# Kernel tuning notes

Hardware: AMD Instinct MI355X
Metric: run time of the kernel (lower is better)

## Reference

```python
import jax, jax.numpy as jnp
import numpy as np

H = 8  # number of heads


def setup_inputs() -> dict:
    key = jax.random.key(0)
    ks = jax.random.split(key, 8)
    B, L, S, D, P = 4, 2048, 2048, 1024, 1024
    sc = 0.02
    return {
        "queries": jax.random.normal(ks[0], (B, L, D), jnp.float32),
        "keys": jax.random.normal(ks[1], (B, S, D), jnp.float32),
        "values": jax.random.normal(ks[2], (B, S, D), jnp.float32),
        "Wq": jax.random.normal(ks[3], (D, P), jnp.float32) * sc,
        "bq": jnp.zeros((P,), jnp.float32),
        "Wk": jax.random.normal(ks[4], (D, P), jnp.float32) * sc,
        "bk": jnp.zeros((P,), jnp.float32),
        "Wv": jax.random.normal(ks[5], (D, P), jnp.float32) * sc,
        "bv": jnp.zeros((P,), jnp.float32),
        "Wo": jax.random.normal(ks[6], (P, D), jnp.float32) * sc,
        "bo": jnp.zeros((D,), jnp.float32),
    }


def reference(queries, keys, values, Wq, bq, Wk, bk, Wv, bv, Wo, bo):
    B, L, _ = queries.shape
    S = keys.shape[1]
    # linear projections, split into heads: [B, T, H, E]
    q = (queries @ Wq + bq).reshape(B, L, H, -1)
    k = (keys @ Wk + bk).reshape(B, S, H, -1)
    v = (values @ Wv + bv).reshape(B, S, H, -1)
    E = q.shape[-1]
    scale = 1.0 / jnp.sqrt(jnp.float32(E))
    scores = jnp.einsum("blhe,bshe->bhls", q, k)
    A = jax.nn.softmax(scale * scores, axis=-1)  # dropout is identity at eval
    V = jnp.einsum("bhls,bshd->blhd", A, v)
    out = V.reshape(B, L, -1)
    return out @ Wo + bo
```

## Files before the change

### kernel.cpp

```cpp
#include <hip/hip_runtime.h>
#include <hip/hip_bf16.h>
#include <cstdint>

typedef __attribute__((ext_vector_type(4))) float f32x4;
typedef __attribute__((ext_vector_type(16))) float f32x16;
typedef __attribute__((ext_vector_type(8))) __bf16 bf16x8;
typedef __attribute__((ext_vector_type(4))) unsigned u32x4;

#define SCALE_Q 0.12751744f

__device__ __forceinline__ short bf16b(float f) {
  unsigned u = __builtin_bit_cast(unsigned, f);
  unsigned r = (u + 0x7fffu + ((u >> 16) & 1u)) >> 16;
  return (short)r;
}

__device__ __forceinline__ unsigned packbf(float lo, float hi) {
  unsigned r;
  asm("v_cvt_pk_bf16_f32 %0, %1, %2" : "=v"(r) : "v"(lo), "v"(hi));
  return r;
}

__device__ __forceinline__ float exp2fast(float x) {
  float r;
  asm("v_exp_f32 %0, %1" : "=v"(r) : "v"(x));
  return r;
}

__device__ __forceinline__ f32x4 mfma16(bf16x8 a, bf16x8 b, f32x4 c) {
  return __builtin_amdgcn_mfma_f32_16x16x32_bf16(a, b, c, 0, 0, 0);
}
__device__ __forceinline__ f32x16 mfma32(bf16x8 a, bf16x8 b, f32x16 c) {
  return __builtin_amdgcn_mfma_f32_32x32x16_bf16(a, b, c, 0, 0, 0);
}

__device__ __forceinline__ void async16(void* lds, const void* g) {
  __builtin_amdgcn_global_load_lds(
      (const __attribute__((address_space(1))) unsigned int*)g,
      (__attribute__((address_space(3))) unsigned int*)lds, 16, 0, 0);
}

__global__ void cvt_x(const float* __restrict__ q, const float* __restrict__ k,
                      const float* __restrict__ v, short* __restrict__ out) {
  const float* src = (blockIdx.y == 0) ? q : (blockIdx.y == 1 ? k : v);
  short* dst = out + (size_t)blockIdx.y * 8388608;
  size_t i = (size_t)blockIdx.x * 256 + threadIdx.x;
  float4 f = reinterpret_cast<const float4*>(src)[i];
  short4 o;
  o.x = bf16b(f.x); o.y = bf16b(f.y); o.z = bf16b(f.z); o.w = bf16b(f.w);
  reinterpret_cast<short4*>(dst)[i] = o;
}

__global__ void cvt_w(const float* __restrict__ Wq, const float* __restrict__ Wk,
                      const float* __restrict__ Wv, const float* __restrict__ Wo,
                      short* __restrict__ out) {
  int z = blockIdx.z;
  const float* W = (z == 0) ? Wq : (z == 1) ? Wk : (z == 2) ? Wv : Wo;
  float scale = (z == 0) ? SCALE_Q : 1.0f;
  __shared__ float t[64][65];
  int n0 = blockIdx.x * 64, k0 = blockIdx.y * 64;
  int c = threadIdx.x & 63, r0 = threadIdx.x >> 6;
#pragma unroll
  for (int rr = 0; rr < 16; ++rr) {
    int r = rr * 4 + r0;
    t[r][c] = W[(size_t)(k0 + r) * 1024 + n0 + c];
  }
  __syncthreads();
  short* dst = out + (size_t)z * 1048576;
#pragma unroll
  for (int rr = 0; rr < 16; ++rr) {
    int r = rr * 4 + r0;
    dst[(size_t)(n0 + r) * 1024 + k0 + c] = bf16b(t[c][r] * scale);
  }
}

__global__ __launch_bounds__(256, 4) void gemm128(
    const short* __restrict__ Ab, const short* __restrict__ WT,
    const float* __restrict__ bq, const float* __restrict__ bk,
    const float* __restrict__ bv, const float* __restrict__ bo,
    short* __restrict__ Qg, short* __restrict__ Kg, short* __restrict__ Vtg,
    float* __restrict__ Out, int zbase, int nwg) {
  __shared__ __align__(16) short LDSbuf[16384];
  short* As = LDSbuf;
  short* Bs = LDSbuf + 8192;

  int cpx = nwg >> 3;
  int swz = ((int)blockIdx.x & 7) * cpx + ((int)blockIdx.x >> 3);
  int z, rem;
  if (zbase == 0) { z = swz >> 9; rem = swz & 511; }
  else { z = 3; rem = swz; }
  int m0 = (rem >> 3) * 128, n0 = (rem & 7) * 128;

  const short* A = (zbase == 0) ? Ab + (size_t)z * 8388608 : Ab;
  const short* Bn = WT + (size_t)z * 1048576;

  int tid = threadIdx.x;
  int lane = tid & 63, wave = tid >> 6;
  int wr = wave >> 1, wc = wave & 1, l15 = lane & 15, lg = lane >> 4;

  f32x4 acc[4][4];
#pragma unroll
  for (int mt = 0; mt < 4; ++mt)
#pragma unroll
    for (int nt = 0; nt < 4; ++nt) acc[mt][nt] = f32x4{0.f, 0.f, 0.f, 0.f};

  for (int k0 = 0; k0 < 1024; k0 += 64) {
#pragma unroll
    for (int i = 0; i < 4; ++i) {
      int r = (tid >> 3) + i * 32, c = tid & 7;
      int gc = c ^ (r & 7);
      async16((char*)As + i * 4096 + tid * 16,
              (const char*)A + ((size_t)(m0 + r) * 1024 + k0) * 2 + gc * 16);
      async16((char*)Bs + i * 4096 + tid * 16,
              (const char*)Bn + ((size_t)(n0 + r) * 1024 + k0) * 2 + gc * 16);
    }
    __syncthreads();
#pragma unroll
    for (int kk = 0; kk < 2; ++kk) {
      bf16x8 a[4], b[4];
#pragma unroll
      for (int mt = 0; mt < 4; ++mt) {
        int r = wr * 64 + mt * 16 + l15;
        a[mt] = *(const bf16x8*)((const char*)As + r * 128 +
                                 ((lg * 16 + kk * 64) ^ ((r & 7) << 4)));
      }
#pragma unroll
      for (int nt = 0; nt < 4; ++nt) {
        int r = wc * 64 + nt * 16 + l15;
        b[nt] = *(const bf16x8*)((const char*)Bs + r * 128 +
                                 ((lg * 16 + kk * 64) ^ ((r & 7) << 4)));
      }
#pragma unroll
      for (int mt = 0; mt < 4; ++mt)
#pragma unroll
        for (int nt = 0; nt < 4; ++nt)
          acc[mt][nt] = mfma16(a[mt], b[nt], acc[mt][nt]);
    }
    __syncthreads();
  }

  if (z == 2) {
    unsigned* Lt = (unsigned*)LDSbuf;
    int b_ = m0 >> 11, h_ = n0 >> 7;
    size_t bh = (size_t)b_ * 8 + h_;
    int sbase = m0 & 2047;
#pragma unroll
    for (int p = 0; p < 2; ++p) {
      if (wc == p) {
#pragma unroll
        for (int nt = 0; nt < 4; ++nt) {
          int el = nt * 16 + l15;
          float bb = bv[n0 + p * 64 + el];
#pragma unroll
          for (int mt = 0; mt < 4; ++mt) {
            int sw = wr * 32 + mt * 8 + lg * 2;
            unsigned lo = packbf(acc[mt][nt][0] + bb, acc[mt][nt][1] + bb);
            unsigned hi = packbf(acc[mt][nt][2] + bb, acc[mt][nt][3] + bb);
            *(uint2*)&Lt[el * 68 + sw] = make_uint2(lo, hi);
          }
        }
      }
      asm volatile("s_waitcnt lgkmcnt(0)" ::: "memory");
      __builtin_amdgcn_s_barrier();
      {
        int row = tid >> 2, ch = tid & 3;
        int e_ = p * 64 + row;
        int sx = ((e_ >> 1) & 7) << 3;
#pragma unroll
        for (int i = 0; i < 4; ++i) {
          int w = ch * 16 + i * 4;
          u32x4 val = *(const u32x4*)&Lt[row * 68 + w];
          int sb = (sbase + w * 2) ^ sx;
          *(u32x4*)&Vtg[(bh * 128 + e_) * 2048 + sb] = val;
        }
      }
      asm volatile("s_waitcnt lgkmcnt(0)" ::: "memory");
      __builtin_amdgcn_s_barrier();
    }
  } else {
#pragma unroll
    for (int mt = 0; mt < 4; ++mt)
#pragma unroll
      for (int nt = 0; nt < 4; ++nt) {
        int n = n0 + wc * 64 + nt * 16 + l15;
        float bb = (z == 0)   ? bq[n] * SCALE_Q
                   : (z == 1) ? bk[n]
                              : bo[n];
#pragma unroll
        for (int j = 0; j < 4; ++j) {
          int m = m0 + wr * 64 + mt * 16 + lg * 4 + j;
          float cv = acc[mt][nt][j] + bb;
          if (z == 3) {
            Out[(size_t)m * 1024 + n] = cv;
          } else {
            short o = bf16b(cv);
            int s_ = m & 2047, b_ = m >> 11, h_ = n >> 7, e_ = n & 127;
            size_t bh = (size_t)b_ * 8 + h_;
            if (z == 0)
              Qg[(bh * 2048 + s_) * 128 + e_] = o;
            else
              Kg[(bh * 2048 + s_) * 128 + (e_ ^ ((s_ & 15) << 3))] = o;
          }
        }
      }
  }
}

__global__ __launch_bounds__(256, 2) void attn(const short* __restrict__ Qg,
                                               const short* __restrict__ Kg,
                                               const short* __restrict__ Vtg,
                                               short* __restrict__ Ctx) {
  __shared__ short Ks[2][8192];
  __shared__ short Vs[2][8192];
  int tid = threadIdx.x;
  int lane = tid & 63, wave = tid >> 6;
  int l31 = lane & 31, h = lane >> 5;
  int bid = blockIdx.x;
  int swz = (bid & 7) * 64 + (bid >> 3);
  int bh = swz >> 4, qb = swz & 15;
  int qbase = qb * 128 + wave * 32;
  const short* Qp = Qg + (size_t)bh * 2048 * 128;
  const char* Kbase = (const char*)(Kg + (size_t)bh * 2048 * 128);
  const char* Vbase = (const char*)(Vtg + (size_t)bh * 128 * 2048);

  auto stage = [&](int t, int buf) {
    int s0 = t * 64;
    char* kd = (char*)&Ks[buf][0];
    char* vd = (char*)&Vs[buf][0];
#pragma unroll
    for (int i = 0; i < 4; ++i)
      async16(kd + i * 4096 + tid * 16,
              Kbase + (size_t)s0 * 256 + i * 4096 + tid * 16);
#pragma unroll
    for (int i = 0; i < 4; ++i) {
      int e = i * 32 + 2 * (tid >> 4) + ((tid >> 3) & 1);
      async16(vd + i * 4096 + tid * 16,
              Vbase + (size_t)e * 4096 + s0 * 2 + (tid & 7) * 16);
    }
  };

  stage(0, 0);

  bf16x8 qa[8];
  const short* qrow = Qp + (size_t)(qbase + l31) * 128 + h * 8;
#pragma unroll
  for (int ksl = 0; ksl < 8; ++ksl) qa[ksl] = *(const bf16x8*)(qrow + ksl * 16);

  f32x16 acc[4];
#pragma unroll
  for (int i = 0; i < 4; ++i)
#pragma unroll
    for (int r = 0; r < 16; ++r) acc[i][r] = 0.f;
  float mrun = -1e30f, lrun = 0.f;

  int swK = (l31 & 15) << 3;
  int swV = ((l31 >> 1) & 7) << 3;

  for (int t = 0; t < 32; ++t) {
    int cur = t & 1;
    if (t < 31) {
      stage(t + 1, cur ^ 1);
      asm volatile("s_waitcnt vmcnt(8)" ::: "memory");
    } else {
      asm volatile("s_waitcnt vmcnt(0)" ::: "memory");
    }
    __builtin_amdgcn_s_barrier();

    const short* Kc = Ks[cur];
    const short* Vc = Vs[cur];

    f32x16 st0, st1;
#pragma unroll
    for (int r = 0; r < 16; ++r) { st0[r] = 0.f; st1[r] = 0.f; }
    __builtin_amdgcn_s_setprio(1);
#pragma unroll
    for (int ksl = 0; ksl < 8; ++ksl) {
      int col = (ksl * 16 + h * 8) ^ swK;
      bf16x8 ka0 = *(const bf16x8*)&Kc[l31 * 128 + col];
      bf16x8 ka1 = *(const bf16x8*)&Kc[(32 + l31) * 128 + col];
      st0 = mfma32(ka0, qa[ksl], st0);
      st1 = mfma32(ka1, qa[ksl], st1);
    }
    __builtin_amdgcn_s_setprio(0);

    float m8[8];
#pragma unroll
    for (int r = 0; r < 8; ++r)
      m8[r] = fmaxf(fmaxf(st0[r], st0[r + 8]), fmaxf(st1[r], st1[r + 8]));
    float mx = fmaxf(fmaxf(fmaxf(m8[0], m8[1]), fmaxf(m8[2], m8[3])),
                     fmaxf(fmaxf(m8[4], m8[5]), fmaxf(m8[6], m8[7])));
    mx = fmaxf(mx, __shfl_xor(mx, 32));
    int skip = __all(mx - mrun <= 7.0f);
    float mn = mrun, sf = 1.f;
    if (!skip) {
      mn = fmaxf(mrun, mx);
      sf = exp2fast(mrun - mn);
      mrun = mn;
    }
#pragma unroll
    for (int r = 0; r < 16; ++r) { st0[r] = exp2fast(st0[r] - mn); }
#pragma unroll
    for (int r = 0; r < 16; ++r) { st1[r] = exp2fast(st1[r] - mn); }
    float s8[8];
#pragma unroll
    for (int r = 0; r < 8; ++r)
      s8[r] = (st0[r] + st0[r + 8]) + (st1[r] + st1[r + 8]);
    float rs = ((s8[0] + s8[1]) + (s8[2] + s8[3])) +
               ((s8[4] + s8[5]) + (s8[6] + s8[7]));
    rs += __shfl_xor(rs, 32);
    if (!skip) {
      lrun = lrun * sf + rs;
#pragma unroll
      for (int reg = 0; reg < 16; ++reg) {
        float s4 = __shfl(sf, (reg & 3) + 8 * (reg >> 2) + 4 * h);
#pragma unroll
        for (int nte = 0; nte < 4; ++nte) acc[nte][reg] *= s4;
      }
    } else {
      lrun += rs;
    }

    unsigned w0[8], w1[8];
#pragma unroll
    for (int m = 0; m < 8; ++m) {
      w0[m] = packbf(st0[2 * m], st0[2 * m + 1]);
      w1[m] = packbf(st1[2 * m], st1[2 * m + 1]);
    }
    bf16x8 pa[4];
#pragma unroll
    for (int ks = 0; ks < 4; ++ks) {
      const unsigned* w = (ks & 2) ? w1 : w0;
      int mb = (ks & 1) * 4;
      unsigned a0 = w[mb], b0 = w[mb + 2];
      unsigned a1 = w[mb + 1], b1 = w[mb + 3];
      asm volatile("v_permlane32_swap_b32 %0, %1" : "+v"(a0), "+v"(b0));
      asm volatile("v_permlane32_swap_b32 %0, %1" : "+v"(a1), "+v"(b1));
      u32x4 tt;
      tt[0] = a0; tt[1] = a1; tt[2] = b0; tt[3] = b1;
      pa[ks] = __builtin_bit_cast(bf16x8, tt);
    }

    __builtin_amdgcn_s_setprio(1);
#pragma unroll
    for (int nte = 0; nte < 4; ++nte) {
      int rbase = (nte * 16 + (l31 >> 1)) * 128 + (lane & 1) * 64;
#pragma unroll
      for (int ks = 0; ks < 4; ++ks) {
        int colk = (ks * 16 + h * 8) ^ swV;
        bf16x8 vb = *(const bf16x8*)&Vc[rbase + colk];
        acc[nte] = mfma32(pa[ks], vb, acc[nte]);
      }
    }
    __builtin_amdgcn_s_setprio(0);
    __builtin_amdgcn_s_barrier();
  }

  float inv = 1.0f / lrun;
  int b_ = bh >> 3, h_ = bh & 7;
#pragma unroll
  for (int reg = 0; reg < 16; ++reg) {
    int qr = (reg & 3) + 8 * (reg >> 2) + 4 * h;
    float iq = __shfl(inv, qr);
    int q = qbase + qr;
    short* orow = Ctx + (((size_t)b_ * 2048 + q) * 8 + h_) * 128;
#pragma unroll
    for (int nte = 0; nte < 4; ++nte)
      orow[nte * 32 + l31] = bf16b(acc[nte][reg] * iq);
  }
}

extern "C" void kernel_launch(void* const* d_in, const int* in_sizes, int n_in,
                              void* d_out, int out_size, void* d_ws, size_t ws_size,
                              hipStream_t stream) {
  const float* q = (const float*)d_in[0];
  const float* k = (const float*)d_in[1];
  const float* v = (const float*)d_in[2];
  const float* Wq = (const float*)d_in[3];
  const float* bq = (const float*)d_in[4];
  const float* Wk = (const float*)d_in[5];
  const float* bk = (const float*)d_in[6];
  const float* Wv = (const float*)d_in[7];
  const float* bv = (const float*)d_in[8];
  const float* Wo = (const float*)d_in[9];
  const float* bo = (const float*)d_in[10];
  float* out = (float*)d_out;

  short* ws = (short*)d_ws;
  short* X3 = ws;
  short* WT = X3 + (size_t)3 * 8388608;
  short* Qg = WT + (size_t)4 * 1048576;
  short* Kg = Qg + (size_t)8388608;
  short* Vtg = Kg + (size_t)8388608;
  short* Ctx = X3;

  hipLaunchKernelGGL(cvt_x, dim3(8192, 3), dim3(256), 0, stream, q, k, v, X3);
  hipLaunchKernelGGL(cvt_w, dim3(16, 16, 4), dim3(256), 0, stream, Wq, Wk, Wv, Wo, WT);
  hipLaunchKernelGGL(gemm128, dim3(1536), dim3(256), 0, stream, X3, WT, bq, bk, bv,
                     bo, Qg, Kg, Vtg, out, 0, 1536);
  hipLaunchKernelGGL(attn, dim3(512), dim3(256), 0, stream, Qg, Kg, Vtg, Ctx);
  hipLaunchKernelGGL(gemm128, dim3(512), dim3(256), 0, stream, Ctx, WT, bq, bk, bv,
                     bo, Qg, Kg, Vtg, out, 3, 512);
}
```

Measured before the change: 192.9 us.

## Double-buffer LDS tiles in projection GEMM to overlap global loads with MFMA

The projection GEMM now keeps two LDS buffers for A and B tiles and issues the async loads for the next K-step before computing the current one, waiting with explicit vmcnt counts instead of a full syncthreads. This is meant to hide global-memory latency behind the MFMA work. LDS use doubles to 64KB per block, which may reduce occupancy below the launch-bounds target of 4 blocks per CU. The epilogue's transpose staging reuses the first A buffer.

```diff
diff --git a/kernel.cpp b/kernel.cpp
--- a/kernel.cpp
+++ b/kernel.cpp
@@ -80,9 +80,7 @@
     const float* __restrict__ bv, const float* __restrict__ bo,
     short* __restrict__ Qg, short* __restrict__ Kg, short* __restrict__ Vtg,
     float* __restrict__ Out, int zbase, int nwg) {
-  __shared__ __align__(16) short LDSbuf[16384];
-  short* As = LDSbuf;
-  short* Bs = LDSbuf + 8192;
+  __shared__ __align__(16) short As[2][8192], Bs[2][8192];
 
   int cpx = nwg >> 3;
   int swz = ((int)blockIdx.x & 7) * cpx + ((int)blockIdx.x >> 3);
@@ -98,36 +96,51 @@
   int lane = tid & 63, wave = tid >> 6;
   int wr = wave >> 1, wc = wave & 1, l15 = lane & 15, lg = lane >> 4;
 
-  f32x4 acc[4][4];
-#pragma unroll
-  for (int mt = 0; mt < 4; ++mt)
-#pragma unroll
-    for (int nt = 0; nt < 4; ++nt) acc[mt][nt] = f32x4{0.f, 0.f, 0.f, 0.f};
-
-  for (int k0 = 0; k0 < 1024; k0 += 64) {
+  auto stage = [&](int t) {
+    int buf = t & 1, k0 = t * 64;
 #pragma unroll
     for (int i = 0; i < 4; ++i) {
       int r = (tid >> 3) + i * 32, c = tid & 7;
       int gc = c ^ (r & 7);
-      async16((char*)As + i * 4096 + tid * 16,
+      async16((char*)&As[buf][0] + i * 4096 + tid * 16,
               (const char*)A + ((size_t)(m0 + r) * 1024 + k0) * 2 + gc * 16);
-      async16((char*)Bs + i * 4096 + tid * 16,
+      async16((char*)&Bs[buf][0] + i * 4096 + tid * 16,
               (const char*)Bn + ((size_t)(n0 + r) * 1024 + k0) * 2 + gc * 16);
     }
-    __syncthreads();
+  };
+
+  f32x4 acc[4][4];
+#pragma unroll
+  for (int mt = 0; mt < 4; ++mt)
+#pragma unroll
+    for (int nt = 0; nt < 4; ++nt) acc[mt][nt] = f32x4{0.f, 0.f, 0.f, 0.f};
+
+  stage(0);
+
+  for (int t = 0; t < 16; ++t) {
+    if (t < 15) {
+      stage(t + 1);
+      asm volatile("s_waitcnt vmcnt(8)" ::: "memory");
+    } else {
+      asm volatile("s_waitcnt vmcnt(0)" ::: "memory");
+    }
+    __builtin_amdgcn_s_barrier();
+
+    const char* Ac = (const char*)&As[t & 1][0];
+    const char* Bc = (const char*)&Bs[t & 1][0];
 #pragma unroll
     for (int kk = 0; kk < 2; ++kk) {
       bf16x8 a[4], b[4];
 #pragma unroll
       for (int mt = 0; mt < 4; ++mt) {
         int r = wr * 64 + mt * 16 + l15;
-        a[mt] = *(const bf16x8*)((const char*)As + r * 128 +
+        a[mt] = *(const bf16x8*)(Ac + r * 128 +
                                  ((lg * 16 + kk * 64) ^ ((r & 7) << 4)));
       }
 #pragma unroll
       for (int nt = 0; nt < 4; ++nt) {
         int r = wc * 64 + nt * 16 + l15;
-        b[nt] = *(const bf16x8*)((const char*)Bs + r * 128 +
+        b[nt] = *(const bf16x8*)(Bc + r * 128 +
                                  ((lg * 16 + kk * 64) ^ ((r & 7) << 4)));
       }
 #pragma unroll
@@ -136,11 +149,11 @@
         for (int nt = 0; nt < 4; ++nt)
           acc[mt][nt] = mfma16(a[mt], b[nt], acc[mt][nt]);
     }
-    __syncthreads();
+    __builtin_amdgcn_s_barrier();
   }
 
   if (z == 2) {
-    unsigned* Lt = (unsigned*)LDSbuf;
+    unsigned* Lt = (unsigned*)&As[0][0];
     int b_ = m0 >> 11, h_ = n0 >> 7;
     size_t bh = (size_t)b_ * 8 + h_;
     int sbase = m0 & 2047;
```

After: 208.0 us. +7.9%, slower.
